# Kernel tuning notes

Hardware: AMD Instinct MI355X
Metric: run time of the kernel (lower is better)

The kernel has to match this reference:

```python
import jax, jax.numpy as jnp
import numpy as np
from math import factorial as fact

L_MAX = 3
K = 128
N = 8192

# ---- Clebsch-Gordan coefficients (Racah formula, real for integer l) ----

def _cg_coeff(l1, m1, l2, m2, l3, m3):
    if m1 + m2 != m3:
        return 0.0
    pref = ((2 * l3 + 1) * fact(l3 + l1 - l2) * fact(l3 - l1 + l2)
            * fact(l1 + l2 - l3) / fact(l1 + l2 + l3 + 1)) ** 0.5
    pref *= (fact(l3 + m3) * fact(l3 - m3) * fact(l1 - m1) * fact(l1 + m1)
             * fact(l2 - m2) * fact(l2 + m2)) ** 0.5
    s = 0.0
    for k in range(max(0, l2 - l3 - m1, l1 - l3 + m2),
                   min(l1 + l2 - l3, l1 - m1, l2 + m2) + 1):
        s += (-1) ** k / (fact(k) * fact(l1 + l2 - l3 - k) * fact(l1 - m1 - k)
                          * fact(l2 + m2 - k) * fact(l3 - l2 + m1 + k)
                          * fact(l3 - l1 - m2 + k))
    return pref * s


def _cg_tensor(l1, l2, l3):
    C = np.zeros((2 * l1 + 1, 2 * l2 + 1, 2 * l3 + 1), dtype=np.float32)
    for m1 in range(-l1, l1 + 1):
        for m2 in range(-l2, l2 + 1):
            m3 = m1 + m2
            if -l3 <= m3 <= l3:
                C[m1 + l1, m2 + l2, m3 + l3] = _cg_coeff(l1, m1, l2, m2, l3, m3)
    return jnp.asarray(C)

# all allowed (l1, l2, l3) coupling paths, deterministic order
PATHS = [(l1, l2, l3)
         for l1 in range(L_MAX + 1)
         for l2 in range(L_MAX + 1)
         for l3 in range(abs(l1 - l2), min(l1 + l2, L_MAX) + 1)]
CG = {p: _cg_tensor(*p) for p in PATHS}
N_PATHS = [sum(1 for p in PATHS if p[2] == l3) for l3 in range(L_MAX + 1)]  # [4,9,11,10]


def setup_inputs() -> dict:
    key = jax.random.key(0)
    ks = jax.random.split(key, 12)
    inp = {}
    for i, l in enumerate(range(L_MAX + 1)):
        inp[f"f1_l{l}"] = jax.random.normal(ks[i], (N, 2 * l + 1, K), jnp.float32)
        inp[f"f2_l{l}"] = jax.random.normal(ks[4 + i], (N, 2 * l + 1, K), jnp.float32)
        fan_in = N_PATHS[l] * K
        inp[f"W_l{l}"] = jax.random.normal(ks[8 + i], (fan_in, K), jnp.float32) / np.sqrt(fan_in)
    return inp


def _forward(f1, f2, W):
    # CG tensor product: per-path contraction, channel-wise in k
    tp = [[] for _ in range(L_MAX + 1)]
    for (l1, l2, l3) in PATHS:
        C = CG[(l1, l2, l3)]  # [2l1+1, 2l2+1, 2l3+1]
        tp[l3].append(jnp.einsum('abm,nak,nbk->nmk', C, f1[l1], f2[l2]))
    # concat paths along channels, linear mix back to K, residual add
    outs = []
    for l3 in range(L_MAX + 1):
        cat = jnp.concatenate(tp[l3], axis=-1)        # [N, 2l3+1, n_paths*K]
        mixed = jnp.einsum('nmp,pk->nmk', cat, W[l3])  # [N, 2l3+1, K]
        outs.append(f1[l3] + mixed)
    return tuple(outs)


def reference(f1_l0, f1_l1, f1_l2, f1_l3,
              f2_l0, f2_l1, f2_l2, f2_l3,
              W_l0, W_l1, W_l2, W_l3):
    f1 = [f1_l0, f1_l1, f1_l2, f1_l3]
    f2 = [f2_l0, f2_l1, f2_l2, f2_l3]
    W = [W_l0, W_l1, W_l2, W_l3]
    return _forward(f1, f2, W)
```

## Files before the change

### kernel.cpp

```cpp
#include <hip/hip_runtime.h>

#define K_DIM 128

typedef __attribute__((ext_vector_type(8))) short short8;
typedef __attribute__((ext_vector_type(4))) float f32x4;

constexpr int C_L1[34] = {0,0,0,0, 1,1,1,1,1,1,1,1,1, 2,2,2,2,2,2,2,2,2,2,2, 3,3,3,3,3,3,3,3,3,3};
constexpr int C_L2[34] = {0,1,2,3, 0,1,1,1,2,2,2,3,3, 0,1,1,1,2,2,2,2,3,3,3, 0,1,1,2,2,2,3,3,3,3};
constexpr int C_L3[34] = {0,1,2,3, 1,0,1,2,1,2,3,2,3, 2,1,2,3,0,1,2,3,1,2,3, 3,2,3,1,2,3,0,1,2,3};
constexpr int C_NP[4]  = {4,9,11,10};
constexpr int C_PL[4][11] = {
  {0,5,17,30, 0,0,0,0,0,0,0},
  {1,4,6,8,14,18,21,27,31, 0,0},
  {2,7,9,11,13,15,19,22,25,28,32},
  {3,10,12,16,20,23,24,26,29,33, 0}
};
constexpr int C_CSUM[4] = {0,8,26,48};
constexpr size_t FOFF[4] = {0, 1048576, 4194304, 9437184};
constexpr int FSZ[4] = {1048576, 3145728, 5242880, 7340032};
constexpr size_t FTOT = 16777216;

__device__ double dfactd(int n){ double r=1.0; for(int i=2;i<=n;++i) r*=(double)i; return r; }

__device__ __forceinline__ unsigned short f2bf(float x) {
    unsigned int b = __float_as_uint(x);
    return (unsigned short)((b + 0x7FFFu + ((b >> 16) & 1u)) >> 16);
}
__device__ __forceinline__ float bflo(unsigned int u){ return __uint_as_float(u << 16); }
__device__ __forceinline__ float bfhi(unsigned int u){ return __uint_as_float(u & 0xFFFF0000u); }

__device__ __forceinline__ unsigned int cvtpk(float lo, float hi) {
    unsigned int r;
    asm("v_cvt_pk_bf16_f32 %0, %1, %2" : "=v"(r) : "v"(lo), "v"(hi));
    return r;
}

__global__ void cg_init(float* __restrict__ C2) {
    int e = blockIdx.x*blockDim.x + threadIdx.x;
    if (e >= 34*49) return;
    int p = e/49, r = e%49, m1i = r/7, m2i = r%7;
    int l1 = C_L1[p], l2 = C_L2[p], l3 = C_L3[p];
    float val = 0.f;
    if (m1i < 2*l1+1 && m2i < 2*l2+1) {
        int m1 = m1i-l1, m2 = m2i-l2, m3 = m1+m2;
        if (m3 >= -l3 && m3 <= l3) {
            double pref = sqrt((double)(2*l3+1) * dfactd(l3+l1-l2)*dfactd(l3-l1+l2)
                               * dfactd(l1+l2-l3) / dfactd(l1+l2+l3+1));
            pref *= sqrt(dfactd(l3+m3)*dfactd(l3-m3)*dfactd(l1-m1)*dfactd(l1+m1)
                         *dfactd(l2-m2)*dfactd(l2+m2));
            int kmin = max(0, max(l2-l3-m1, l1-l3+m2));
            int kmax = min(l1+l2-l3, min(l1-m1, l2+m2));
            double s = 0.0;
            for (int k=kmin;k<=kmax;++k) {
                double t = dfactd(k)*dfactd(l1+l2-l3-k)*dfactd(l1-m1-k)
                         * dfactd(l2+m2-k)*dfactd(l3-l2+m1+k)*dfactd(l3-l1-m2+k);
                s += ((k&1)? -1.0:1.0)/t;
            }
            val = (float)(pref*s);
        }
    }
    C2[e] = val;
}

__global__ void wt_prep(const float* __restrict__ W0, const float* __restrict__ W1,
                        const float* __restrict__ W2, const float* __restrict__ W3,
                        unsigned short* __restrict__ wt) {
    int b = blockIdx.x;
    int chunk = b >> 5;
    int e = ((b & 31) << 8) + threadIdx.x;
    int kk = e & 63, col = e >> 6;
    int l3 = (chunk < 8) ? 0 : (chunk < 26) ? 1 : (chunk < 48) ? 2 : 3;
    int local = chunk - C_CSUM[l3];
    int kin = local*64 + kk;
    const float* W = (l3==0)?W0:(l3==1)?W1:(l3==2)?W2:W3;
    float v = W[(size_t)kin*K_DIM + col];
    wt[(size_t)chunk*8192 + col*64 + (kk ^ ((col&7)<<3))] = f2bf(v);
}

__global__ void fpack(const float* __restrict__ s0, const float* __restrict__ s1,
                      const float* __restrict__ s2, const float* __restrict__ s3,
                      const float* __restrict__ s4, const float* __restrict__ s5,
                      const float* __restrict__ s6, const float* __restrict__ s7,
                      unsigned short* __restrict__ dst) {
    int y = blockIdx.y;
    int l = y & 3, fi = y >> 2;
    const float* srcs[8] = {s0,s1,s2,s3,s4,s5,s6,s7};
    const float* src = srcs[y];
    int i4 = blockIdx.x*256 + threadIdx.x;
    if (i4*4 >= FSZ[l]) return;
    float4 v = reinterpret_cast<const float4*>(src)[i4];
    unsigned int u0 = (unsigned int)f2bf(v.x) | ((unsigned int)f2bf(v.y) << 16);
    unsigned int u1 = (unsigned int)f2bf(v.z) | ((unsigned int)f2bf(v.w) << 16);
    unsigned short* d = dst + fi*FTOT + FOFF[l] + (size_t)i4*4;
    *reinterpret_cast<uint2*>(d) = make_uint2(u0, u1);
}

template<int L3, int PI>
__device__ __forceinline__ void tp_into(
    const unsigned int (&q1)[16][2], const unsigned int (&q2)[16][2],
    const float* __restrict__ C2slot, unsigned char* __restrict__ Ab,
    int nodel, int chq)
{
    constexpr int P  = C_PL[L3][PI];
    constexpr int l1 = C_L1[P], l2 = C_L2[P];
    constexpr int d1 = 2*l1+1, d2 = 2*l2+1;
    constexpr int TL3 = 2*L3+1;
    #pragma unroll
    for (int h=0; h<2; ++h) {
        float xlo[d1], xhi[d1];
        #pragma unroll
        for (int m=0;m<d1;++m) { xlo[m]=bflo(q1[l1*l1+m][h]); xhi[m]=bfhi(q1[l1*l1+m][h]); }
        float a[TL3][2];
        #pragma unroll
        for (int mt=0;mt<TL3;++mt){ a[mt][0]=0.f; a[mt][1]=0.f; }
        #pragma unroll
        for (int m2i=0; m2i<d2; ++m2i) {
            float y0 = bflo(q2[l2*l2+m2i][h]);
            float y1 = bfhi(q2[l2*l2+m2i][h]);
            #pragma unroll
            for (int m1i=0; m1i<d1; ++m1i) {
                int mt = (m1i-l1) + (m2i-l2) + L3;
                if (mt >= 0 && mt < TL3) {
                    float c = C2slot[m1i*7 + m2i];
                    a[mt][0] = fmaf(c*xlo[m1i], y0, a[mt][0]);
                    a[mt][1] = fmaf(c*xhi[m1i], y1, a[mt][1]);
                }
            }
        }
        #pragma unroll
        for (int mt=0; mt<TL3; ++mt) {
            int row = nodel*TL3 + mt;
            *reinterpret_cast<unsigned int*>(
                Ab + row*256 + h*128 + ((chq*4) ^ ((row&7)<<4))) = cvtpk(a[mt][0], a[mt][1]);
        }
    }
}

template<int L3, int PI>
__device__ __forceinline__ void load_wf(const unsigned short* __restrict__ wt,
                                        int col, int lg, short8 (&wf)[4]) {
    const int wkey = (col&7)<<4;
    const unsigned char* wb0 = (const unsigned char*)(wt + (size_t)(C_CSUM[L3] + PI*2    )*8192);
    const unsigned char* wb1 = (const unsigned char*)(wt + (size_t)(C_CSUM[L3] + PI*2 + 1)*8192);
    wf[0] = *reinterpret_cast<const short8*>(wb0 + col*128 + ((16*lg     ) ^ wkey));
    wf[1] = *reinterpret_cast<const short8*>(wb0 + col*128 + ((16*lg + 64) ^ wkey));
    wf[2] = *reinterpret_cast<const short8*>(wb1 + col*128 + ((16*lg     ) ^ wkey));
    wf[3] = *reinterpret_cast<const short8*>(wb1 + col*128 + ((16*lg + 64) ^ wkey));
}

template<int L3>
__device__ __forceinline__ void mfma_from(
    const unsigned char* __restrict__ Ab, const short8 (&wf)[4],
    int lr, int lg, f32x4 (&cacc)[2*L3+1])
{
    constexpr int TL3 = 2*L3+1;
    #pragma unroll
    for (int kst=0; kst<4; ++kst) {
        #pragma unroll
        for (int rt=0; rt<TL3; ++rt) {
            int arow = 16*rt + lr;
            short8 af = *reinterpret_cast<const short8*>(
                Ab + arow*256 + ((16*lg + 64*kst) ^ ((arow&7)<<4)));
            cacc[rt] = __builtin_amdgcn_mfma_f32_16x16x32_bf16(af, wf[kst], cacc[rt], 0, 0, 0);
        }
    }
}

template<int L3, int PI>
__device__ __forceinline__ void pipe(
    const unsigned int (&q1)[16][2], const unsigned int (&q2)[16][2],
    const unsigned short* __restrict__ wt, const float* __restrict__ C2,
    float (&C2s)[2][49], unsigned char* A0, unsigned char* A1,
    int tid, int nodel, int chq, int col, int lr, int lg, f32x4 (&cacc)[2*L3+1])
{
    constexpr int NP = C_NP[L3];
    short8 wf[4];
    load_wf<L3, PI>(wt, col, lg, wf);
    if constexpr (PI+2 < NP) {
        if (tid < 49) C2s[PI&1][tid] = C2[C_PL[L3][PI+2]*49 + tid];
    }
    if constexpr (PI+1 < NP)
        tp_into<L3, PI+1>(q1, q2, C2s[(PI+1)&1], ((PI+1)&1) ? A1 : A0, nodel, chq);
    mfma_from<L3>((PI&1) ? A1 : A0, wf, lr, lg, cacc);
    __syncthreads();
    if constexpr (PI+1 < NP)
        pipe<L3, PI+1>(q1, q2, wt, C2, C2s, A0, A1, tid, nodel, chq, col, lr, lg, cacc);
}

template<int L3>
__device__ __forceinline__ void run16(
    int n0,
    const unsigned short* __restrict__ f1b, const unsigned short* __restrict__ f2b,
    const unsigned short* __restrict__ wt, const float* __restrict__ C2,
    float* __restrict__ out, float (&C2s)[2][49], unsigned char* Asb)
{
    constexpr int TL3 = 2*L3+1;
    constexpr int NP  = C_NP[L3];
    const int tid   = threadIdx.x;
    const int nodel = tid >> 5;
    const int chq   = tid & 31;
    const int lane  = tid & 63, wid = tid >> 6;
    const int lr    = lane & 15, lg = lane >> 4;
    const int col   = 16*wid + lr;
    constexpr size_t OB = FOFF[L3];
    unsigned char* A0 = Asb;
    unsigned char* A1 = Asb + 28672;

    unsigned int q1[16][2], q2[16][2];
    #pragma unroll
    for (int l=0; l<4; ++l) {
        const unsigned short* g1 = f1b + FOFF[l] + (size_t)(n0+nodel)*((2*l+1)*128) + chq*2;
        const unsigned short* g2 = f2b + FOFF[l] + (size_t)(n0+nodel)*((2*l+1)*128) + chq*2;
        #pragma unroll
        for (int m=0; m<2*l+1; ++m) {
            #pragma unroll
            for (int h=0; h<2; ++h) {
                q1[l*l+m][h] = *reinterpret_cast<const unsigned int*>(g1 + m*128 + h*64);
                q2[l*l+m][h] = *reinterpret_cast<const unsigned int*>(g2 + m*128 + h*64);
            }
        }
    }

    f32x4 cacc[TL3];
    #pragma unroll
    for (int rt=0; rt<TL3; ++rt) cacc[rt] = (f32x4){0.f,0.f,0.f,0.f};

    if (tid < 49) {
        C2s[0][tid] = C2[C_PL[L3][0]*49 + tid];
        if constexpr (NP > 1) C2s[1][tid] = C2[C_PL[L3][1]*49 + tid];
    }
    __syncthreads();
    tp_into<L3, 0>(q1, q2, C2s[0], A0, nodel, chq);
    __syncthreads();
    pipe<L3, 0>(q1, q2, wt, C2, C2s, A0, A1, tid, nodel, chq, col, lr, lg, cacc);

    float* S = reinterpret_cast<float*>(Asb);
    const unsigned short* __restrict__ fr = f1b + OB;
    #pragma unroll
    for (int rt0=0; rt0<TL3; rt0+=4) {
        const int bn = (TL3 - rt0 < 4) ? (TL3 - rt0) : 4;
        #pragma unroll
        for (int rtl=0; rtl<4; ++rtl) {
            if (rtl < bn) {
                #pragma unroll
                for (int i=0;i<4;++i)
                    S[(rtl*16 + 4*lg + i)*132 + col] = cacc[rt0+rtl][i];
            }
        }
        __syncthreads();
        #pragma unroll
        for (int it=0; it<4; ++it) {
            if (it < bn) {
                int s = tid + it*512;
                int rows = s >> 5, cq = (s & 31) * 4;
                int gr = n0*TL3 + (rt0 + (rows >> 4))*16 + (rows & 15);
                size_t ro = (size_t)gr * K_DIM;
                float4 v = *reinterpret_cast<const float4*>(&S[rows*132 + cq]);
                uint2 rb = *reinterpret_cast<const uint2*>(fr + ro + cq);
                v.x += bflo(rb.x); v.y += bfhi(rb.x);
                v.z += bflo(rb.y); v.w += bfhi(rb.y);
                *reinterpret_cast<float4*>(&out[OB + ro + cq]) = v;
            }
        }
        __syncthreads();
    }
}

__global__ __launch_bounds__(512, 2) void cg_main(
    const unsigned short* __restrict__ f1b, const unsigned short* __restrict__ f2b,
    const unsigned short* __restrict__ wt,
    const float* __restrict__ C2, float* __restrict__ out)
{
    __shared__ __align__(16) unsigned char Asb[2*28672];
    __shared__ float C2s[2][49];

    int bid = blockIdx.x;
    int x = bid & 7, j = bid >> 3;
    int rnd = j >> 4, k = j & 15;
    int l3 = k >> 2, q = k & 3;
    int n0 = x*1024 + rnd*64 + q*16;
    if (l3 == 0)      run16<0>(n0, f1b, f2b, wt, C2, out, C2s, Asb);
    else if (l3 == 1) run16<1>(n0, f1b, f2b, wt, C2, out, C2s, Asb);
    else if (l3 == 2) run16<2>(n0, f1b, f2b, wt, C2, out, C2s, Asb);
    else              run16<3>(n0, f1b, f2b, wt, C2, out, C2s, Asb);
}

extern "C" void kernel_launch(void* const* d_in, const int* in_sizes, int n_in,
                              void* d_out, int out_size, void* d_ws, size_t ws_size,
                              hipStream_t stream) {
    const float* f10 = (const float*)d_in[0];
    const float* f20 = (const float*)d_in[1];
    const float* W0  = (const float*)d_in[2];
    const float* f11 = (const float*)d_in[3];
    const float* f21 = (const float*)d_in[4];
    const float* W1  = (const float*)d_in[5];
    const float* f12 = (const float*)d_in[6];
    const float* f22 = (const float*)d_in[7];
    const float* W2  = (const float*)d_in[8];
    const float* f13 = (const float*)d_in[9];
    const float* f23 = (const float*)d_in[10];
    const float* W3  = (const float*)d_in[11];

    float* C2 = (float*)d_ws;
    unsigned short* wtw = (unsigned short*)((char*)d_ws + 8192);
    unsigned short* f1b = (unsigned short*)((char*)d_ws + 1122304);
    unsigned short* f2b = f1b + FTOT;
    float* out = (float*)d_out;

    hipLaunchKernelGGL(cg_init, dim3(7), dim3(256), 0, stream, C2);
    hipLaunchKernelGGL(wt_prep, dim3(68*32), dim3(256), 0, stream, W0, W1, W2, W3, wtw);
    hipLaunchKernelGGL(fpack, dim3(7168, 8), dim3(256), 0, stream,
        f10, f11, f12, f13, f20, f21, f22, f23, f1b);
    hipLaunchKernelGGL(cg_main, dim3(2048), dim3(512), 0, stream,
        f1b, f2b, wtw, C2, out);
}
```

Measured before the change: 159.6 us.

## Shrink blocks to 8 nodes with padded rows and stream f2 per path

The main kernel moves from 512-thread blocks handling 16 nodes to 256-thread blocks handling 8 nodes, with launch bounds raised to four blocks per CU. Each wave now computes two output column tiles. The A tile rows are padded to an even count per node (with a zero row), so the MFMA row tiles drop to L3+1, though part of the work runs on zero padding. The f2 slices are reloaded from global memory for each path instead of being kept in registers for all l. The goal is lower register and LDS pressure and higher occupancy, at the cost of redundant global loads of f2 and wasted MFMA work on the padded rows.

```diff
diff --git a/kernel.cpp b/kernel.cpp
--- a/kernel.cpp
+++ b/kernel.cpp
@@ -97,7 +97,7 @@
 
 template<int L3, int PI>
 __device__ __forceinline__ void tp_into(
-    const unsigned int (&q1)[16][2], const unsigned int (&q2)[16][2],
+    const unsigned int (&q1)[16][2], const unsigned int (&q2s)[7][2],
     const float* __restrict__ C2slot, unsigned char* __restrict__ Ab,
     int nodel, int chq)
 {
@@ -105,184 +105,214 @@
     constexpr int l1 = C_L1[P], l2 = C_L2[P];
     constexpr int d1 = 2*l1+1, d2 = 2*l2+1;
     constexpr int TL3 = 2*L3+1;
+    constexpr int STR = TL3+1;
     #pragma unroll
     for (int h=0; h<2; ++h) {
-        float xlo[d1], xhi[d1];
-        #pragma unroll
-        for (int m=0;m<d1;++m) { xlo[m]=bflo(q1[l1*l1+m][h]); xhi[m]=bfhi(q1[l1*l1+m][h]); }
         float a[TL3][2];
         #pragma unroll
         for (int mt=0;mt<TL3;++mt){ a[mt][0]=0.f; a[mt][1]=0.f; }
         #pragma unroll
         for (int m2i=0; m2i<d2; ++m2i) {
-            float y0 = bflo(q2[l2*l2+m2i][h]);
-            float y1 = bfhi(q2[l2*l2+m2i][h]);
+            float y0 = bflo(q2s[m2i][h]);
+            float y1 = bfhi(q2s[m2i][h]);
             #pragma unroll
             for (int m1i=0; m1i<d1; ++m1i) {
                 int mt = (m1i-l1) + (m2i-l2) + L3;
                 if (mt >= 0 && mt < TL3) {
                     float c = C2slot[m1i*7 + m2i];
-                    a[mt][0] = fmaf(c*xlo[m1i], y0, a[mt][0]);
-                    a[mt][1] = fmaf(c*xhi[m1i], y1, a[mt][1]);
+                    a[mt][0] = fmaf(c*bflo(q1[l1*l1+m1i][h]), y0, a[mt][0]);
+                    a[mt][1] = fmaf(c*bfhi(q1[l1*l1+m1i][h]), y1, a[mt][1]);
                 }
             }
         }
         #pragma unroll
         for (int mt=0; mt<TL3; ++mt) {
-            int row = nodel*TL3 + mt;
+            int row = nodel*STR + mt;
             *reinterpret_cast<unsigned int*>(
-                Ab + row*256 + h*128 + ((chq*4) ^ ((row&7)<<4))) = cvtpk(a[mt][0], a[mt][1]);
+                Ab + row*256 + ((h*128 + chq*4) ^ ((row&7)<<4))) = cvtpk(a[mt][0], a[mt][1]);
+        }
+        {
+            int row = nodel*STR + TL3;
+            *reinterpret_cast<unsigned int*>(
+                Ab + row*256 + ((h*128 + chq*4) ^ ((row&7)<<4))) = 0u;
         }
     }
 }
 
 template<int L3, int PI>
 __device__ __forceinline__ void load_wf(const unsigned short* __restrict__ wt,
-                                        int col, int lg, short8 (&wf)[4]) {
-    const int wkey = (col&7)<<4;
+                                        int wid, int lr, int lg, short8 (&wf)[2][4]) {
     const unsigned char* wb0 = (const unsigned char*)(wt + (size_t)(C_CSUM[L3] + PI*2    )*8192);
     const unsigned char* wb1 = (const unsigned char*)(wt + (size_t)(C_CSUM[L3] + PI*2 + 1)*8192);
-    wf[0] = *reinterpret_cast<const short8*>(wb0 + col*128 + ((16*lg     ) ^ wkey));
-    wf[1] = *reinterpret_cast<const short8*>(wb0 + col*128 + ((16*lg + 64) ^ wkey));
-    wf[2] = *reinterpret_cast<const short8*>(wb1 + col*128 + ((16*lg     ) ^ wkey));
-    wf[3] = *reinterpret_cast<const short8*>(wb1 + col*128 + ((16*lg + 64) ^ wkey));
+    #pragma unroll
+    for (int j=0;j<2;++j) {
+        int col = 16*(2*wid+j) + lr;
+        int wkey = (col&7)<<4;
+        wf[j][0] = *reinterpret_cast<const short8*>(wb0 + col*128 + ((16*lg     ) ^ wkey));
+        wf[j][1] = *reinterpret_cast<const short8*>(wb0 + col*128 + ((16*lg + 64) ^ wkey));
+        wf[j][2] = *reinterpret_cast<const short8*>(wb1 + col*128 + ((16*lg     ) ^ wkey));
+        wf[j][3] = *reinterpret_cast<const short8*>(wb1 + col*128 + ((16*lg + 64) ^ wkey));
+    }
 }
 
 template<int L3>
 __device__ __forceinline__ void mfma_from(
-    const unsigned char* __restrict__ Ab, const short8 (&wf)[4],
-    int lr, int lg, f32x4 (&cacc)[2*L3+1])
-{
-    constexpr int TL3 = 2*L3+1;
+    const unsigned char* __restrict__ Ab, const short8 (&wf)[2][4],
+    int lr, int lg, f32x4 (&acc)[2][L3+1])
+{
+    constexpr int RT = L3+1;
     #pragma unroll
     for (int kst=0; kst<4; ++kst) {
         #pragma unroll
-        for (int rt=0; rt<TL3; ++rt) {
+        for (int rt=0; rt<RT; ++rt) {
             int arow = 16*rt + lr;
             short8 af = *reinterpret_cast<const short8*>(
                 Ab + arow*256 + ((16*lg + 64*kst) ^ ((arow&7)<<4)));
-            cacc[rt] = __builtin_amdgcn_mfma_f32_16x16x32_bf16(af, wf[kst], cacc[rt], 0, 0, 0);
-        }
+            acc[0][rt] = __builtin_amdgcn_mfma_f32_16x16x32_bf16(af, wf[0][kst], acc[0][rt], 0, 0, 0);
+            acc[1][rt] = __builtin_amdgcn_mfma_f32_16x16x32_bf16(af, wf[1][kst], acc[1][rt], 0, 0, 0);
+        }
+    }
+}
+
+template<int L3, int PI>
+__device__ __forceinline__ void stream_f2(
+    const unsigned short* __restrict__ f2b, int n0, int nodel, int chq,
+    unsigned int (&q2s)[7][2])
+{
+    constexpr int P  = C_PL[L3][PI];
+    constexpr int l2 = C_L2[P];
+    constexpr int d2 = 2*l2+1;
+    const unsigned short* g2 = f2b + FOFF[l2] + (size_t)(n0+nodel)*(d2*128) + chq*2;
+    #pragma unroll
+    for (int m=0;m<d2;++m) {
+        q2s[m][0] = *reinterpret_cast<const unsigned int*>(g2 + m*128);
+        q2s[m][1] = *reinterpret_cast<const unsigned int*>(g2 + m*128 + 64);
     }
 }
 
 template<int L3, int PI>
 __device__ __forceinline__ void pipe(
-    const unsigned int (&q1)[16][2], const unsigned int (&q2)[16][2],
+    const unsigned int (&q1)[16][2], unsigned int (&q2s)[7][2],
+    const unsigned short* __restrict__ f2b,
     const unsigned short* __restrict__ wt, const float* __restrict__ C2,
     float (&C2s)[2][49], unsigned char* A0, unsigned char* A1,
-    int tid, int nodel, int chq, int col, int lr, int lg, f32x4 (&cacc)[2*L3+1])
+    int tid, int n0, int nodel, int chq, int wid, int lr, int lg,
+    f32x4 (&acc)[2][L3+1])
 {
     constexpr int NP = C_NP[L3];
-    short8 wf[4];
-    load_wf<L3, PI>(wt, col, lg, wf);
+    short8 wf[2][4];
+    load_wf<L3, PI>(wt, wid, lr, lg, wf);
     if constexpr (PI+2 < NP) {
         if (tid < 49) C2s[PI&1][tid] = C2[C_PL[L3][PI+2]*49 + tid];
     }
-    if constexpr (PI+1 < NP)
-        tp_into<L3, PI+1>(q1, q2, C2s[(PI+1)&1], ((PI+1)&1) ? A1 : A0, nodel, chq);
-    mfma_from<L3>((PI&1) ? A1 : A0, wf, lr, lg, cacc);
+    if constexpr (PI+1 < NP) {
+        stream_f2<L3, PI+1>(f2b, n0, nodel, chq, q2s);
+        tp_into<L3, PI+1>(q1, q2s, C2s[(PI+1)&1], ((PI+1)&1) ? A1 : A0, nodel, chq);
+    }
+    mfma_from<L3>((PI&1) ? A1 : A0, wf, lr, lg, acc);
     __syncthreads();
     if constexpr (PI+1 < NP)
-        pipe<L3, PI+1>(q1, q2, wt, C2, C2s, A0, A1, tid, nodel, chq, col, lr, lg, cacc);
+        pipe<L3, PI+1>(q1, q2s, f2b, wt, C2, C2s, A0, A1,
+                       tid, n0, nodel, chq, wid, lr, lg, acc);
 }
 
 template<int L3>
-__device__ __forceinline__ void run16(
+__device__ __forceinline__ void run8(
     int n0,
     const unsigned short* __restrict__ f1b, const unsigned short* __restrict__ f2b,
     const unsigned short* __restrict__ wt, const float* __restrict__ C2,
     float* __restrict__ out, float (&C2s)[2][49], unsigned char* Asb)
 {
     constexpr int TL3 = 2*L3+1;
+    constexpr int STR = TL3+1;
+    constexpr int RT  = L3+1;
     constexpr int NP  = C_NP[L3];
     const int tid   = threadIdx.x;
     const int nodel = tid >> 5;
     const int chq   = tid & 31;
     const int lane  = tid & 63, wid = tid >> 6;
     const int lr    = lane & 15, lg = lane >> 4;
-    const int col   = 16*wid + lr;
     constexpr size_t OB = FOFF[L3];
     unsigned char* A0 = Asb;
-    unsigned char* A1 = Asb + 28672;
-
-    unsigned int q1[16][2], q2[16][2];
+    unsigned char* A1 = Asb + 16384;
+
+    unsigned int q1[16][2];
     #pragma unroll
     for (int l=0; l<4; ++l) {
         const unsigned short* g1 = f1b + FOFF[l] + (size_t)(n0+nodel)*((2*l+1)*128) + chq*2;
-        const unsigned short* g2 = f2b + FOFF[l] + (size_t)(n0+nodel)*((2*l+1)*128) + chq*2;
         #pragma unroll
         for (int m=0; m<2*l+1; ++m) {
-            #pragma unroll
-            for (int h=0; h<2; ++h) {
-                q1[l*l+m][h] = *reinterpret_cast<const unsigned int*>(g1 + m*128 + h*64);
-                q2[l*l+m][h] = *reinterpret_cast<const unsigned int*>(g2 + m*128 + h*64);
-            }
-        }
-    }
-
-    f32x4 cacc[TL3];
-    #pragma unroll
-    for (int rt=0; rt<TL3; ++rt) cacc[rt] = (f32x4){0.f,0.f,0.f,0.f};
+            q1[l*l+m][0] = *reinterpret_cast<const unsigned int*>(g1 + m*128);
+            q1[l*l+m][1] = *reinterpret_cast<const unsigned int*>(g1 + m*128 + 64);
+        }
+    }
+    unsigned int q2s[7][2];
+
+    f32x4 acc[2][RT];
+    #pragma unroll
+    for (int j=0;j<2;++j)
+        #pragma unroll
+        for (int rt=0; rt<RT; ++rt) acc[j][rt] = (f32x4){0.f,0.f,0.f,0.f};
 
     if (tid < 49) {
         C2s[0][tid] = C2[C_PL[L3][0]*49 + tid];
         if constexpr (NP > 1) C2s[1][tid] = C2[C_PL[L3][1]*49 + tid];
     }
     __syncthreads();
-    tp_into<L3, 0>(q1, q2, C2s[0], A0, nodel, chq);
+    stream_f2<L3, 0>(f2b, n0, nodel, chq, q2s);
+    tp_into<L3, 0>(q1, q2s, C2s[0], A0, nodel, chq);
     __syncthreads();
-    pipe<L3, 0>(q1, q2, wt, C2, C2s, A0, A1, tid, nodel, chq, col, lr, lg, cacc);
+    pipe<L3, 0>(q1, q2s, f2b, wt, C2, C2s, A0, A1,
+                tid, n0, nodel, chq, wid, lr, lg, acc);
 
     float* S = reinterpret_cast<float*>(Asb);
     const unsigned short* __restrict__ fr = f1b + OB;
     #pragma unroll
-    for (int rt0=0; rt0<TL3; rt0+=4) {
-        const int bn = (TL3 - rt0 < 4) ? (TL3 - rt0) : 4;
-        #pragma unroll
-        for (int rtl=0; rtl<4; ++rtl) {
-            if (rtl < bn) {
-                #pragma unroll
-                for (int i=0;i<4;++i)
-                    S[(rtl*16 + 4*lg + i)*132 + col] = cacc[rt0+rtl][i];
-            }
-        }
-        __syncthreads();
-        #pragma unroll
-        for (int it=0; it<4; ++it) {
-            if (it < bn) {
-                int s = tid + it*512;
-                int rows = s >> 5, cq = (s & 31) * 4;
-                int gr = n0*TL3 + (rt0 + (rows >> 4))*16 + (rows & 15);
-                size_t ro = (size_t)gr * K_DIM;
-                float4 v = *reinterpret_cast<const float4*>(&S[rows*132 + cq]);
-                uint2 rb = *reinterpret_cast<const uint2*>(fr + ro + cq);
-                v.x += bflo(rb.x); v.y += bfhi(rb.x);
-                v.z += bflo(rb.y); v.w += bfhi(rb.y);
-                *reinterpret_cast<float4*>(&out[OB + ro + cq]) = v;
-            }
-        }
-        __syncthreads();
-    }
-}
-
-__global__ __launch_bounds__(512, 2) void cg_main(
+    for (int j=0;j<2;++j) {
+        int col = 16*(2*wid+j) + lr;
+        #pragma unroll
+        for (int rt=0; rt<RT; ++rt)
+            #pragma unroll
+            for (int i=0;i<4;++i)
+                S[(16*rt + 4*lg + i)*132 + col] = acc[j][rt][i];
+    }
+    __syncthreads();
+    constexpr int RR = 8*TL3;
+    #pragma unroll
+    for (int it=0; it*256 < RR*32; ++it) {
+        int s = tid + it*256;
+        if (s < RR*32) {
+            int rr = s >> 5, cq = (s & 31) * 4;
+            int nd = rr / TL3;
+            int mt = rr - nd*TL3;
+            int prow = nd*STR + mt;
+            size_t ro = (size_t)((n0+nd)*TL3 + mt) * K_DIM;
+            float4 v = *reinterpret_cast<const float4*>(&S[prow*132 + cq]);
+            uint2 rb = *reinterpret_cast<const uint2*>(fr + ro + cq);
+            v.x += bflo(rb.x); v.y += bfhi(rb.x);
+            v.z += bflo(rb.y); v.w += bfhi(rb.y);
+            *reinterpret_cast<float4*>(&out[OB + ro + cq]) = v;
+        }
+    }
+}
+
+__global__ __launch_bounds__(256, 4) void cg_main(
     const unsigned short* __restrict__ f1b, const unsigned short* __restrict__ f2b,
     const unsigned short* __restrict__ wt,
     const float* __restrict__ C2, float* __restrict__ out)
 {
-    __shared__ __align__(16) unsigned char Asb[2*28672];
+    __shared__ __align__(16) unsigned char Asb[34304];
     __shared__ float C2s[2][49];
 
     int bid = blockIdx.x;
     int x = bid & 7, j = bid >> 3;
-    int rnd = j >> 4, k = j & 15;
-    int l3 = k >> 2, q = k & 3;
-    int n0 = x*1024 + rnd*64 + q*16;
-    if (l3 == 0)      run16<0>(n0, f1b, f2b, wt, C2, out, C2s, Asb);
-    else if (l3 == 1) run16<1>(n0, f1b, f2b, wt, C2, out, C2s, Asb);
-    else if (l3 == 2) run16<2>(n0, f1b, f2b, wt, C2, out, C2s, Asb);
-    else              run16<3>(n0, f1b, f2b, wt, C2, out, C2s, Asb);
+    int rnd = j >> 3, k = j & 7;
+    int l3 = k >> 1, q = k & 1;
+    int n0 = x*1024 + rnd*16 + q*8;
+    if (l3 == 0)      run8<0>(n0, f1b, f2b, wt, C2, out, C2s, Asb);
+    else if (l3 == 1) run8<1>(n0, f1b, f2b, wt, C2, out, C2s, Asb);
+    else if (l3 == 2) run8<2>(n0, f1b, f2b, wt, C2, out, C2s, Asb);
+    else              run8<3>(n0, f1b, f2b, wt, C2, out, C2s, Asb);
 }
 
 extern "C" void kernel_launch(void* const* d_in, const int* in_sizes, int n_in,
@@ -311,6 +341,6 @@
     hipLaunchKernelGGL(wt_prep, dim3(68*32), dim3(256), 0, stream, W0, W1, W2, W3, wtw);
     hipLaunchKernelGGL(fpack, dim3(7168, 8), dim3(256), 0, stream,
         f10, f11, f12, f13, f20, f21, f22, f23, f1b);
-    hipLaunchKernelGGL(cg_main, dim3(2048), dim3(512), 0, stream,
+    hipLaunchKernelGGL(cg_main, dim3(4096), dim3(256), 0, stream,
         f1b, f2b, wtw, C2, out);
 }
```

Result: slower. 374.7 us (+134.8%).
